# Kernel optimization log

Hardware: AMD Instinct MI355X
Metric: run time of the kernel (lower is better)

## Reference

```python
import jax, jax.numpy as jnp
import numpy as np

B, T, D_MODEL = 1, 2048, 2048
N_HEADS, N_KV_HEADS, HEAD_DIM = 32, 8, 64
N_REP = N_HEADS // N_KV_HEADS
ROPE_THETA = 10000.0


def setup_inputs() -> dict:
    key = jax.random.key(0)
    ks = jax.random.split(key, 5)
    x = jax.random.normal(ks[0], (B, T, D_MODEL), dtype=jnp.float32)
    # rotary frequencies: complex exp stored as (cos, sin) pairs -> [T, HEAD_DIM//2, 2]
    inv_freq = 1.0 / (ROPE_THETA ** (jnp.arange(0, HEAD_DIM, 2, dtype=jnp.float32) / HEAD_DIM))
    angles = jnp.arange(T, dtype=jnp.float32)[:, None] * inv_freq[None, :]  # [T, HEAD_DIM//2]
    freqs_cis = jnp.stack([jnp.cos(angles), jnp.sin(angles)], axis=-1)  # [T, HD/2, 2]
    s = 1.0 / np.sqrt(D_MODEL)
    wq = jax.random.normal(ks[1], (D_MODEL, N_HEADS * HEAD_DIM), dtype=jnp.float32) * s
    wk = jax.random.normal(ks[2], (D_MODEL, N_KV_HEADS * HEAD_DIM), dtype=jnp.float32) * s
    wv = jax.random.normal(ks[3], (D_MODEL, N_KV_HEADS * HEAD_DIM), dtype=jnp.float32) * s
    wo = jax.random.normal(ks[4], (N_HEADS * HEAD_DIM, D_MODEL), dtype=jnp.float32) * (1.0 / np.sqrt(N_HEADS * HEAD_DIM))
    return {"x": x, "freqs_cis": freqs_cis, "wq": wq, "wk": wk, "wv": wv, "wo": wo}


def _apply_rotary(t, freqs_cis):
    # t: [B, T, H, D]; freqs_cis: [T, D//2, 2] as (cos, sin). Complex multiply.
    tr = t.astype(jnp.float32).reshape(*t.shape[:-1], -1, 2)  # [B,T,H,D/2,2]
    re, im = tr[..., 0], tr[..., 1]
    cos = freqs_cis[None, :, None, :, 0]  # [1,T,1,D/2]
    sin = freqs_cis[None, :, None, :, 1]
    out_re = re * cos - im * sin
    out_im = re * sin + im * cos
    out = jnp.stack([out_re, out_im], axis=-1).reshape(t.shape)
    return out.astype(t.dtype)


def reference(x, freqs_cis, wq, wk, wv, wo):
    Bx, Tx, _ = x.shape
    q = (x @ wq).reshape(Bx, Tx, N_HEADS, HEAD_DIM)
    k = (x @ wk).reshape(Bx, Tx, N_KV_HEADS, HEAD_DIM)
    v = (x @ wv).reshape(Bx, Tx, N_KV_HEADS, HEAD_DIM)
    q = _apply_rotary(q, freqs_cis)
    k = _apply_rotary(k, freqs_cis)
    # GQA: group query heads, broadcast against kv heads (no repeat materialization)
    qg = q.transpose(0, 2, 1, 3).reshape(Bx, N_KV_HEADS, N_REP, Tx, HEAD_DIM)  # [B,G,R,T,D]
    kg = k.transpose(0, 2, 1, 3)  # [B,G,T,D]
    vg = v.transpose(0, 2, 1, 3)  # [B,G,T,D]
    scale = 1.0 / np.sqrt(HEAD_DIM)
    scores = jnp.einsum('bgrtd,bgsd->bgrts', qg, kg) * scale  # [B,G,R,T,T]
    causal = jnp.tril(jnp.ones((Tx, Tx), dtype=bool))
    scores = jnp.where(causal, scores, jnp.finfo(scores.dtype).min)
    p = jax.nn.softmax(scores, axis=-1)
    y = jnp.einsum('bgrts,bgsd->bgrtd', p, vg)  # [B,G,R,T,D]
    y = y.reshape(Bx, N_HEADS, Tx, HEAD_DIM).transpose(0, 2, 1, 3).reshape(Bx, Tx, N_HEADS * HEAD_DIM)
    return y @ wo
```

## Files before the change

### kernel.cpp

```cpp
#include <hip/hip_runtime.h>
#include <hip/hip_bf16.h>
#include <stdint.h>
#include <stddef.h>

#define T_SEQ 2048
#define DMODEL 2048
#define NHEADS 32
#define NKV 8
#define HD 64
#define NQD (NHEADS * HD)
#define NKVD (NKV * HD)
#define QKVN (NQD + 2 * NKVD)

typedef __bf16 bf16_t;
typedef __bf16 bf16x8 __attribute__((ext_vector_type(8)));
typedef __bf16 bf16x4 __attribute__((ext_vector_type(4)));
typedef __bf16 bf16x2 __attribute__((ext_vector_type(2)));
typedef float f32x4 __attribute__((ext_vector_type(4)));

typedef __attribute__((address_space(1))) void gvoid_t;
typedef __attribute__((address_space(3))) void lvoid_t;

__device__ __forceinline__ void gload_lds16(const void* g, void* l) {
  __builtin_amdgcn_global_load_lds((gvoid_t*)g, (lvoid_t*)l, 16, 0, 0);
}

__global__ __launch_bounds__(256) void cast_f32_bf16_kernel(
    const float* __restrict__ in, bf16_t* __restrict__ out, int n8) {
  int i = blockIdx.x * 256 + threadIdx.x;
  if (i >= n8) return;
  const float4* p = (const float4*)in + (size_t)i * 2;
  float4 a = p[0], b = p[1];
  bf16x8 o = {(bf16_t)a.x, (bf16_t)a.y, (bf16_t)a.z, (bf16_t)a.w,
              (bf16_t)b.x, (bf16_t)b.y, (bf16_t)b.z, (bf16_t)b.w};
  *(bf16x8*)(out + (size_t)i * 8) = o;
}

__global__ __launch_bounds__(256) void transpose_cast_kernel(
    const float* __restrict__ in, bf16_t* __restrict__ out,
    int R, int C, int ldin, int ldout) {
  __shared__ float tile[32][33];
  const int c0 = blockIdx.x * 32, r0 = blockIdx.y * 32;
  const int tx = threadIdx.x & 31, ty = threadIdx.x >> 5;
#pragma unroll
  for (int i = 0; i < 32; i += 8)
    tile[ty + i][tx] = in[(size_t)(r0 + ty + i) * ldin + c0 + tx];
  __syncthreads();
#pragma unroll
  for (int i = 0; i < 32; i += 8)
    out[(size_t)(c0 + ty + i) * ldout + r0 + tx] = (bf16_t)tile[tx][ty + i];
}

__global__ __launch_bounds__(256) void rope_cast_kernel(
    const float* __restrict__ src, const float* __restrict__ fc,
    bf16_t* __restrict__ dst, int H, int ldin, float oscale) {
  const int i = blockIdx.x * 256 + threadIdx.x;
  const int npr = H * 32;
  const int t = i / npr;
  const int rem = i - t * npr;
  const int h = rem >> 5, fi = rem & 31;
  const float2 rein = *(const float2*)&src[(size_t)t * ldin + h * 64 + fi * 2];
  const float2 cs = *(const float2*)&fc[((size_t)t * 32 + fi) * 2];
  const float o0 = (rein.x * cs.x - rein.y * cs.y) * oscale;
  const float o1 = (rein.x * cs.y + rein.y * cs.x) * oscale;
  bf16x2 ob = {(bf16_t)o0, (bf16_t)o1};
  *(bf16x2*)&dst[(size_t)t * (H * 64) + h * 64 + fi * 2] = ob;
}

__global__ __launch_bounds__(256) void gemm_bt64_kernel(
    const bf16_t* __restrict__ A, const bf16_t* __restrict__ BT,
    float* __restrict__ C, int M, int N, int K) {
  __shared__ bf16_t As[128 * 64];
  __shared__ bf16_t Bs[64 * 64];
  const int tid = threadIdx.x;
  const int lane = tid & 63;
  const int w = tid >> 6;
  const int lr = lane & 15, lg = lane >> 4;
  const int m0 = blockIdx.y * 128, n0 = blockIdx.x * 64;
  const int wm = (w >> 1) * 64, wn = (w & 1) * 32;

  const bf16_t* gA[4];
  bf16_t* lA[4];
#pragma unroll
  for (int j = 0; j < 4; ++j) {
    const int c = tid + j * 256;
    const int row = c >> 3, cc = c & 7;
    gA[j] = A + (size_t)(m0 + row) * K + ((cc ^ (row & 7)) * 8);
    lA[j] = As + c * 8;
  }
  const bf16_t* gB[2];
  bf16_t* lB[2];
#pragma unroll
  for (int j = 0; j < 2; ++j) {
    const int c = tid + j * 256;
    const int row = c >> 3, cc = c & 7;
    gB[j] = BT + (size_t)(n0 + row) * K + ((cc ^ (row & 7)) * 8);
    lB[j] = Bs + c * 8;
  }

  f32x4 acc[4][2] = {};

  for (int k0 = 0; k0 < K; k0 += 64) {
#pragma unroll
    for (int j = 0; j < 4; ++j) gload_lds16(gA[j] + k0, lA[j]);
#pragma unroll
    for (int j = 0; j < 2; ++j) gload_lds16(gB[j] + k0, lB[j]);
    __syncthreads();
#pragma unroll
    for (int ks = 0; ks < 2; ++ks) {
      bf16x8 af[4], bfr[2];
#pragma unroll
      for (int mi = 0; mi < 4; ++mi) {
        const int row = wm + mi * 16 + lr;
        af[mi] = *(const bf16x8*)((const char*)As + row * 128 +
                                  ((ks * 64 + lg * 16) ^ ((row & 7) << 4)));
      }
#pragma unroll
      for (int nj = 0; nj < 2; ++nj) {
        const int row = wn + nj * 16 + lr;
        bfr[nj] = *(const bf16x8*)((const char*)Bs + row * 128 +
                                   ((ks * 64 + lg * 16) ^ ((row & 7) << 4)));
      }
      __builtin_amdgcn_s_setprio(1);
#pragma unroll
      for (int mi = 0; mi < 4; ++mi)
#pragma unroll
        for (int nj = 0; nj < 2; ++nj)
          acc[mi][nj] = __builtin_amdgcn_mfma_f32_16x16x32_bf16(
              af[mi], bfr[nj], acc[mi][nj], 0, 0, 0);
      __builtin_amdgcn_s_setprio(0);
    }
    __syncthreads();
  }

#pragma unroll
  for (int mi = 0; mi < 4; ++mi)
#pragma unroll
    for (int nj = 0; nj < 2; ++nj) {
      const int row = m0 + wm + mi * 16 + lg * 4;
      const int col = n0 + wn + nj * 16 + lr;
#pragma unroll
      for (int r = 0; r < 4; ++r)
        C[(size_t)(row + r) * N + col] = acc[mi][nj][r];
    }
}

__global__ __launch_bounds__(256) void attn_kernel(
    const bf16_t* __restrict__ Q, const bf16_t* __restrict__ Kb,
    const bf16_t* __restrict__ VT, bf16_t* __restrict__ Y,
    bf16_t* __restrict__ Yp, float* __restrict__ Mb, float* __restrict__ Lb) {
  __shared__ bf16_t Ks[2][64 * 64];
  __shared__ bf16_t Vs[2][64 * 64];
  __shared__ char Pb[4][32 * 128];
  const int bid = blockIdx.x;
  const int kh = bid & 7;
  const int idx = 95 - (bid >> 3);
  int qt, c;
  if (idx < 32) { qt = idx; c = 0; }
  else { const int t2 = idx - 32; qt = 32 + (t2 >> 1); c = t2 & 1; }
  const int nt = (qt + 2) >> 1;
  const bool single = (nt <= 16);
  const int tstart = c * 16;
  const int tend = (c == 0) ? (single ? nt : 16) : nt;

  const int tid = threadIdx.x, lane = tid & 63, w = tid >> 6;
  const int h = kh * 4 + w;
  const int lr = lane & 15, lg = lane >> 4;
  const int q0 = qt * 32;
  char* pb = (char*)Pb[w];
  const int swz = (lr & 7) << 4;

  const int rA = w * 8 + (lane >> 3);
  const int rB = (w + 4) * 8 + (lane >> 3);
  const int ce = (((lane & 7) ^ (lane >> 3)) * 8);
  const bf16_t* kgA = Kb + (size_t)rA * NKVD + kh * HD + ce;
  const bf16_t* kgB = Kb + (size_t)rB * NKVD + kh * HD + ce;
  const bf16_t* vgA = VT + (size_t)(kh * HD + rA) * T_SEQ + ce;
  const bf16_t* vgB = VT + (size_t)(kh * HD + rB) * T_SEQ + ce;
  const int ldA = w * 512 + lane * 8;
  const int ldB = (w + 4) * 512 + lane * 8;

  bf16x8 qf[2][2];
#pragma unroll
  for (int iq = 0; iq < 2; ++iq)
#pragma unroll
    for (int ks = 0; ks < 2; ++ks)
      qf[iq][ks] = *(const bf16x8*)&Q[(size_t)(q0 + iq * 16 + lr) * NQD + h * HD + ks * 32 + lg * 8];

  float m_i[2] = {-1e30f, -1e30f}, l_i[2] = {0.f, 0.f};
  f32x4 acc_o[2][4] = {};

  {
    const size_t ko = (size_t)tstart * 64 * NKVD;
    gload_lds16(kgA + ko, &Ks[0][ldA]);
    gload_lds16(kgB + ko, &Ks[0][ldB]);
    gload_lds16(vgA + tstart * 64, &Vs[0][ldA]);
    gload_lds16(vgB + tstart * 64, &Vs[0][ldB]);
  }
  __syncthreads();

  int cur = 0;
  for (int t = tstart; t < tend; ++t) {
    const int s0 = t * 64;
    if (t + 1 < tend) {
      const size_t ko = (size_t)(s0 + 64) * NKVD;
      gload_lds16(kgA + ko, &Ks[cur ^ 1][ldA]);
      gload_lds16(kgB + ko, &Ks[cur ^ 1][ldB]);
      gload_lds16(vgA + s0 + 64, &Vs[cur ^ 1][ldA]);
      gload_lds16(vgB + s0 + 64, &Vs[cur ^ 1][ldB]);
    }
    const char* kbase = (const char*)&Ks[cur][0];
    const char* vbase = (const char*)&Vs[cur][0];

    bf16x8 kf[4][2];
#pragma unroll
    for (int j = 0; j < 4; ++j)
#pragma unroll
      for (int ks = 0; ks < 2; ++ks)
        kf[j][ks] = *(const bf16x8*)(kbase + (j * 16 + lr) * 128 + ((ks * 64 + lg * 16) ^ swz));

    f32x4 st[2][4] = {};
    __builtin_amdgcn_s_setprio(1);
#pragma unroll
    for (int iq = 0; iq < 2; ++iq)
#pragma unroll
      for (int j = 0; j < 4; ++j)
#pragma unroll
        for (int ks = 0; ks < 2; ++ks)
          st[iq][j] = __builtin_amdgcn_mfma_f32_16x16x32_bf16(kf[j][ks], qf[iq][ks], st[iq][j], 0, 0, 0);
    __builtin_amdgcn_s_setprio(0);

    bf16x8 vf[2][4];
#pragma unroll
    for (int ks = 0; ks < 2; ++ks)
#pragma unroll
      for (int df = 0; df < 4; ++df)
        vf[ks][df] = *(const bf16x8*)(vbase + (df * 16 + lr) * 128 + ((ks * 64 + lg * 16) ^ swz));

    const bool domask = (s0 + 64 > q0);
#pragma unroll
    for (int iq = 0; iq < 2; ++iq) {
      float sv[16];
      const int tq = q0 + iq * 16 + lr;
#pragma unroll
      for (int j = 0; j < 4; ++j)
#pragma unroll
        for (int r = 0; r < 4; ++r) {
          float v = st[iq][j][r];
          if (domask && (s0 + j * 16 + lg * 4 + r > tq)) v = -1e30f;
          sv[j * 4 + r] = v;
        }
      float pm = fmaxf(fmaxf(fmaxf(sv[0], sv[1]), fmaxf(sv[2], sv[3])),
                       fmaxf(fmaxf(sv[4], sv[5]), fmaxf(sv[6], sv[7])));
      float pm2 = fmaxf(fmaxf(fmaxf(sv[8], sv[9]), fmaxf(sv[10], sv[11])),
                        fmaxf(fmaxf(sv[12], sv[13]), fmaxf(sv[14], sv[15])));
      pm = fmaxf(pm, pm2);
      pm = fmaxf(pm, __shfl_xor(pm, 16));
      pm = fmaxf(pm, __shfl_xor(pm, 32));

      if (!__all(pm <= m_i[iq] + 8.0f)) {
        const float mnew = fmaxf(m_i[iq], pm);
        const float es = exp2f(m_i[iq] - mnew);
        m_i[iq] = mnew;
        l_i[iq] *= es;
        float eso[4];
#pragma unroll
        for (int r = 0; r < 4; ++r) eso[r] = __shfl(es, lg * 4 + r);
#pragma unroll
        for (int df = 0; df < 4; ++df)
#pragma unroll
          for (int r = 0; r < 4; ++r) acc_o[iq][df][r] *= eso[r];
      }

      float rs0 = 0.f, rs1 = 0.f;
      bf16_t pe[16];
#pragma unroll
      for (int z = 0; z < 8; ++z) {
        const float p = exp2f(sv[z] - m_i[iq]);
        rs0 += p;
        pe[z] = (bf16_t)p;
      }
#pragma unroll
      for (int z = 8; z < 16; ++z) {
        const float p = exp2f(sv[z] - m_i[iq]);
        rs1 += p;
        pe[z] = (bf16_t)p;
      }
      l_i[iq] += rs0 + rs1;

#pragma unroll
      for (int j = 0; j < 4; ++j) {
        bf16x4 pk = {pe[j * 4 + 0], pe[j * 4 + 1], pe[j * 4 + 2], pe[j * 4 + 3]};
        *(bf16x4*)(pb + (iq * 16 + lr) * 128 + ((j * 32 + lg * 8) ^ swz)) = pk;
      }
    }

    bf16x8 pa[2][2];
#pragma unroll
    for (int iq = 0; iq < 2; ++iq)
#pragma unroll
      for (int ks = 0; ks < 2; ++ks)
        pa[iq][ks] = *(const bf16x8*)(pb + (iq * 16 + lr) * 128 + ((ks * 64 + lg * 16) ^ swz));

    __builtin_amdgcn_s_setprio(1);
#pragma unroll
    for (int iq = 0; iq < 2; ++iq)
#pragma unroll
      for (int df = 0; df < 4; ++df)
#pragma unroll
        for (int ks = 0; ks < 2; ++ks)
          acc_o[iq][df] = __builtin_amdgcn_mfma_f32_16x16x32_bf16(pa[iq][ks], vf[ks][df], acc_o[iq][df], 0, 0, 0);
    __builtin_amdgcn_s_setprio(0);

    __syncthreads();
    cur ^= 1;
  }

  float lts[2];
#pragma unroll
  for (int iq = 0; iq < 2; ++iq) {
    float lt = l_i[iq];
    lt += __shfl_xor(lt, 16);
    lt += __shfl_xor(lt, 32);
    lts[iq] = lt;
  }
  if (single) {
#pragma unroll
    for (int iq = 0; iq < 2; ++iq) {
      float lf[4];
#pragma unroll
      for (int r = 0; r < 4; ++r) lf[r] = __shfl(lts[iq], lg * 4 + r);
#pragma unroll
      for (int r = 0; r < 4; ++r) {
        const float inv = 1.f / lf[r];
        const int t = q0 + iq * 16 + lg * 4 + r;
#pragma unroll
        for (int df = 0; df < 4; ++df)
          Y[(size_t)t * NQD + h * HD + df * 16 + lr] = (bf16_t)(acc_o[iq][df][r] * inv);
      }
    }
  } else {
    const int cid = (kh * 32 + (qt - 32)) * 2 + c;
    bf16_t* yp = Yp + ((size_t)cid * 4 + w) * 2048;
#pragma unroll
    for (int iq = 0; iq < 2; ++iq) {
      float lf[4];
#pragma unroll
      for (int r = 0; r < 4; ++r) lf[r] = __shfl(lts[iq], lg * 4 + r);
#pragma unroll
      for (int r = 0; r < 4; ++r) {
        const float inv = 1.f / lf[r];
        const int q = iq * 16 + lg * 4 + r;
#pragma unroll
        for (int df = 0; df < 4; ++df)
          yp[q * 64 + df * 16 + lr] = (bf16_t)(acc_o[iq][df][r] * inv);
      }
    }
    if (lg == 0) {
#pragma unroll
      for (int iq = 0; iq < 2; ++iq) {
        Mb[cid * 128 + w * 32 + iq * 16 + lr] = m_i[iq];
        Lb[cid * 128 + w * 32 + iq * 16 + lr] = lts[iq];
      }
    }
  }
}

__global__ __launch_bounds__(256) void merge_kernel(
    const bf16_t* __restrict__ Yp, const float* __restrict__ Mb,
    const float* __restrict__ Lb, bf16_t* __restrict__ Y) {
  const int qt = 32 + blockIdx.x, kh = blockIdx.y;
  const int w = threadIdx.x >> 6, lane = threadIdx.x & 63;
  const int h = kh * 4 + w;
  const int cid0 = (kh * 32 + (qt - 32)) * 2, cid1 = cid0 + 1;
  const bf16_t* y0 = Yp + ((size_t)cid0 * 4 + w) * 2048;
  const bf16_t* y1 = Yp + ((size_t)cid1 * 4 + w) * 2048;
#pragma unroll 4
  for (int q = 0; q < 32; ++q) {
    const float m0 = Mb[cid0 * 128 + w * 32 + q];
    const float m1 = Mb[cid1 * 128 + w * 32 + q];
    const float l0 = Lb[cid0 * 128 + w * 32 + q];
    const float l1 = Lb[cid1 * 128 + w * 32 + q];
    const float M = fmaxf(m0, m1);
    const float a0 = exp2f(m0 - M) * l0;
    const float a1 = exp2f(m1 - M) * l1;
    const float inv = 1.f / (a0 + a1);
    const float v0 = (float)y0[q * 64 + lane];
    const float v1 = (float)y1[q * 64 + lane];
    Y[(size_t)(qt * 32 + q) * NQD + h * HD + lane] = (bf16_t)((v0 * a0 + v1 * a1) * inv);
  }
}

extern "C" void kernel_launch(void* const* d_in, const int* in_sizes, int n_in,
                              void* d_out, int out_size, void* d_ws, size_t ws_size,
                              hipStream_t stream) {
  const float* x = (const float*)d_in[0];
  const float* fc = (const float*)d_in[1];
  const float* wq = (const float*)d_in[2];
  const float* wk = (const float*)d_in[3];
  const float* wv = (const float*)d_in[4];
  const float* wo = (const float*)d_in[5];
  float* out = (float*)d_out;
  char* ws = (char*)d_ws;

  bf16_t* xb   = (bf16_t*)(ws + 0);
  bf16_t* wT   = (bf16_t*)(ws + (8u << 20));
  float*  qkvf = (float*)(ws + (20u << 20));
  bf16_t* qb   = (bf16_t*)(ws + (8u << 20));
  bf16_t* kb   = (bf16_t*)(ws + (16u << 20));
  bf16_t* vt   = (bf16_t*)(ws + (18u << 20));
  bf16_t* woT  = (bf16_t*)(ws + (20u << 20));
  bf16_t* yb   = (bf16_t*)(ws + 0);
  bf16_t* Yp   = (bf16_t*)(ws + (28u << 20));
  float*  Mb   = (float*)(ws + (36u << 20));
  float*  Lb   = (float*)(ws + (36u << 20) + (256u << 10));

  const float SCL_Q = 0.18033688011112042f;

  hipLaunchKernelGGL(cast_f32_bf16_kernel, dim3(2048), dim3(256), 0, stream,
                     x, xb, (T_SEQ * DMODEL) / 8);
  hipLaunchKernelGGL(transpose_cast_kernel, dim3(64, 64), dim3(256), 0, stream,
                     wq, wT, DMODEL, NQD, NQD, DMODEL);
  hipLaunchKernelGGL(transpose_cast_kernel, dim3(16, 64), dim3(256), 0, stream,
                     wk, wT + (size_t)NQD * DMODEL, DMODEL, NKVD, NKVD, DMODEL);
  hipLaunchKernelGGL(transpose_cast_kernel, dim3(16, 64), dim3(256), 0, stream,
                     wv, wT + (size_t)(NQD + NKVD) * DMODEL, DMODEL, NKVD, NKVD, DMODEL);
  hipLaunchKernelGGL(gemm_bt64_kernel, dim3(QKVN / 64, T_SEQ / 128), dim3(256), 0, stream,
                     xb, wT, qkvf, T_SEQ, QKVN, DMODEL);
  hipLaunchKernelGGL(rope_cast_kernel, dim3((T_SEQ * NHEADS * 32) / 256), dim3(256), 0, stream,
                     qkvf, fc, qb, NHEADS, QKVN, SCL_Q);
  hipLaunchKernelGGL(rope_cast_kernel, dim3((T_SEQ * NKV * 32) / 256), dim3(256), 0, stream,
                     qkvf + NQD, fc, kb, NKV, QKVN, 1.0f);
  hipLaunchKernelGGL(transpose_cast_kernel, dim3(16, 64), dim3(256), 0, stream,
                     qkvf + NQD + NKVD, vt, T_SEQ, NKVD, QKVN, T_SEQ);
  hipLaunchKernelGGL(transpose_cast_kernel, dim3(64, 64), dim3(256), 0, stream,
                     wo, woT, NQD, DMODEL, DMODEL, NQD);
  hipLaunchKernelGGL(attn_kernel, dim3(768), dim3(256), 0, stream,
                     qb, kb, vt, yb, Yp, Mb, Lb);
  hipLaunchKernelGGL(merge_kernel, dim3(32, 8), dim3(256), 0, stream,
                     Yp, Mb, Lb, yb);
  hipLaunchKernelGGL(gemm_bt64_kernel, dim3(DMODEL / 64, T_SEQ / 128), dim3(256), 0, stream,
                     yb, woT, out, T_SEQ, DMODEL, NQD);
}
```

Baseline: 184.7 us.

## Rebalance causal attention split into 1/2/3 chunks and load V directly from global

Reworks the attention work decomposition so long query tiles are split into three KV chunks, mid tiles into two, and short tiles run whole, with the merge kernel extended to combine up to three partials. V fragments are now read straight from global memory into registers instead of being staged through LDS, which halves shared memory and allows a launch-bounds occupancy hint of four blocks. The partial output buffer is moved into the output tensor, which is later overwritten by the final GEMM. This targets the tail imbalance of causal attention and LDS pressure, at the cost of uncached strided global V reads and more merge work.

After: 258.2 us. 39.8% more time.

```diff
diff --git a/kernel.cpp b/kernel.cpp
--- a/kernel.cpp
+++ b/kernel.cpp
@@ -145,23 +145,23 @@
     }
 }
 
-__global__ __launch_bounds__(256) void attn_kernel(
+__global__ __launch_bounds__(256, 4) void attn_kernel(
     const bf16_t* __restrict__ Q, const bf16_t* __restrict__ Kb,
     const bf16_t* __restrict__ VT, bf16_t* __restrict__ Y,
     bf16_t* __restrict__ Yp, float* __restrict__ Mb, float* __restrict__ Lb) {
   __shared__ bf16_t Ks[2][64 * 64];
-  __shared__ bf16_t Vs[2][64 * 64];
   __shared__ char Pb[4][32 * 128];
   const int bid = blockIdx.x;
   const int kh = bid & 7;
-  const int idx = 95 - (bid >> 3);
-  int qt, c;
-  if (idx < 32) { qt = idx; c = 0; }
-  else { const int t2 = idx - 32; qt = 32 + (t2 >> 1); c = t2 & 1; }
+  const int item = bid >> 3;
+  int qt, c, nc;
+  if (item < 75) { qt = 63 - item / 3; c = item % 3; nc = 3; }
+  else if (item < 115) { const int j = item - 75; qt = 38 - (j >> 1); c = j & 1; nc = 2; }
+  else { qt = 18 - (item - 115); c = 0; nc = 1; }
   const int nt = (qt + 2) >> 1;
-  const bool single = (nt <= 16);
-  const int tstart = c * 16;
-  const int tend = (c == 0) ? (single ? nt : 16) : nt;
+  const int tstart = (nt * c) / nc;
+  const int tend = (nt * (c + 1)) / nc;
+  const bool single = (nc == 1);
 
   const int tid = threadIdx.x, lane = tid & 63, w = tid >> 6;
   const int h = kh * 4 + w;
@@ -170,15 +170,17 @@
   char* pb = (char*)Pb[w];
   const int swz = (lr & 7) << 4;
 
-  const int rA = w * 8 + (lane >> 3);
-  const int rB = (w + 4) * 8 + (lane >> 3);
-  const int ce = (((lane & 7) ^ (lane >> 3)) * 8);
-  const bf16_t* kgA = Kb + (size_t)rA * NKVD + kh * HD + ce;
-  const bf16_t* kgB = Kb + (size_t)rB * NKVD + kh * HD + ce;
-  const bf16_t* vgA = VT + (size_t)(kh * HD + rA) * T_SEQ + ce;
-  const bf16_t* vgB = VT + (size_t)(kh * HD + rB) * T_SEQ + ce;
-  const int ldA = w * 512 + lane * 8;
-  const int ldB = (w + 4) * 512 + lane * 8;
+  const int r1 = tid >> 3, cc1 = tid & 7;
+  const int r2 = r1 + 32;
+  const bf16_t* kg1 = Kb + (size_t)r1 * NKVD + kh * HD + ((cc1 ^ (r1 & 7)) * 8);
+  const bf16_t* kg2 = Kb + (size_t)r2 * NKVD + kh * HD + ((cc1 ^ (r2 & 7)) * 8);
+  const int ld1 = tid * 8, ld2 = tid * 8 + 2048;
+  const size_t kstep = (size_t)64 * NKVD;
+
+  const bf16_t* vp0 = VT + (size_t)(kh * HD + 0 + lr) * T_SEQ + lg * 8 + tstart * 64;
+  const bf16_t* vp1 = VT + (size_t)(kh * HD + 16 + lr) * T_SEQ + lg * 8 + tstart * 64;
+  const bf16_t* vp2 = VT + (size_t)(kh * HD + 32 + lr) * T_SEQ + lg * 8 + tstart * 64;
+  const bf16_t* vp3 = VT + (size_t)(kh * HD + 48 + lr) * T_SEQ + lg * 8 + tstart * 64;
 
   bf16x8 qf[2][2];
 #pragma unroll
@@ -189,29 +191,33 @@
 
   float m_i[2] = {-1e30f, -1e30f}, l_i[2] = {0.f, 0.f};
   f32x4 acc_o[2][4] = {};
-
-  {
-    const size_t ko = (size_t)tstart * 64 * NKVD;
-    gload_lds16(kgA + ko, &Ks[0][ldA]);
-    gload_lds16(kgB + ko, &Ks[0][ldB]);
-    gload_lds16(vgA + tstart * 64, &Vs[0][ldA]);
-    gload_lds16(vgB + tstart * 64, &Vs[0][ldB]);
-  }
+  const f32x4 Z = {0.f, 0.f, 0.f, 0.f};
+
+  size_t koff = (size_t)tstart * kstep;
+  gload_lds16(kg1 + koff, &Ks[0][ld1]);
+  gload_lds16(kg2 + koff, &Ks[0][ld2]);
   __syncthreads();
 
   int cur = 0;
   for (int t = tstart; t < tend; ++t) {
     const int s0 = t * 64;
     if (t + 1 < tend) {
-      const size_t ko = (size_t)(s0 + 64) * NKVD;
-      gload_lds16(kgA + ko, &Ks[cur ^ 1][ldA]);
-      gload_lds16(kgB + ko, &Ks[cur ^ 1][ldB]);
-      gload_lds16(vgA + s0 + 64, &Vs[cur ^ 1][ldA]);
-      gload_lds16(vgB + s0 + 64, &Vs[cur ^ 1][ldB]);
-    }
+      gload_lds16(kg1 + koff + kstep, &Ks[cur ^ 1][ld1]);
+      gload_lds16(kg2 + koff + kstep, &Ks[cur ^ 1][ld2]);
+    }
+    koff += kstep;
+
+    bf16x8 vf[2][4];
+#pragma unroll
+    for (int ks = 0; ks < 2; ++ks) {
+      vf[ks][0] = *(const bf16x8*)(vp0 + ks * 32);
+      vf[ks][1] = *(const bf16x8*)(vp1 + ks * 32);
+      vf[ks][2] = *(const bf16x8*)(vp2 + ks * 32);
+      vf[ks][3] = *(const bf16x8*)(vp3 + ks * 32);
+    }
+    vp0 += 64; vp1 += 64; vp2 += 64; vp3 += 64;
+
     const char* kbase = (const char*)&Ks[cur][0];
-    const char* vbase = (const char*)&Vs[cur][0];
-
     bf16x8 kf[4][2];
 #pragma unroll
     for (int j = 0; j < 4; ++j)
@@ -219,23 +225,16 @@
       for (int ks = 0; ks < 2; ++ks)
         kf[j][ks] = *(const bf16x8*)(kbase + (j * 16 + lr) * 128 + ((ks * 64 + lg * 16) ^ swz));
 
-    f32x4 st[2][4] = {};
+    f32x4 st[2][4];
     __builtin_amdgcn_s_setprio(1);
 #pragma unroll
     for (int iq = 0; iq < 2; ++iq)
 #pragma unroll
-      for (int j = 0; j < 4; ++j)
-#pragma unroll
-        for (int ks = 0; ks < 2; ++ks)
-          st[iq][j] = __builtin_amdgcn_mfma_f32_16x16x32_bf16(kf[j][ks], qf[iq][ks], st[iq][j], 0, 0, 0);
+      for (int j = 0; j < 4; ++j) {
+        st[iq][j] = __builtin_amdgcn_mfma_f32_16x16x32_bf16(kf[j][0], qf[iq][0], Z, 0, 0, 0);
+        st[iq][j] = __builtin_amdgcn_mfma_f32_16x16x32_bf16(kf[j][1], qf[iq][1], st[iq][j], 0, 0, 0);
+      }
     __builtin_amdgcn_s_setprio(0);
-
-    bf16x8 vf[2][4];
-#pragma unroll
-    for (int ks = 0; ks < 2; ++ks)
-#pragma unroll
-      for (int df = 0; df < 4; ++df)
-        vf[ks][df] = *(const bf16x8*)(vbase + (df * 16 + lr) * 128 + ((ks * 64 + lg * 16) ^ swz));
 
     const bool domask = (s0 + 64 > q0);
 #pragma unroll
@@ -340,7 +339,8 @@
       }
     }
   } else {
-    const int cid = (kh * 32 + (qt - 32)) * 2 + c;
+    const int cid = (nc == 3) ? (kh * 115 + 40 + (qt - 39) * 3 + c)
+                              : (kh * 115 + (qt - 19) * 2 + c);
     bf16_t* yp = Yp + ((size_t)cid * 4 + w) * 2048;
 #pragma unroll
     for (int iq = 0; iq < 2; ++iq) {
@@ -369,25 +369,34 @@
 __global__ __launch_bounds__(256) void merge_kernel(
     const bf16_t* __restrict__ Yp, const float* __restrict__ Mb,
     const float* __restrict__ Lb, bf16_t* __restrict__ Y) {
-  const int qt = 32 + blockIdx.x, kh = blockIdx.y;
+  const int qt = 19 + blockIdx.x, kh = blockIdx.y;
   const int w = threadIdx.x >> 6, lane = threadIdx.x & 63;
   const int h = kh * 4 + w;
-  const int cid0 = (kh * 32 + (qt - 32)) * 2, cid1 = cid0 + 1;
-  const bf16_t* y0 = Yp + ((size_t)cid0 * 4 + w) * 2048;
-  const bf16_t* y1 = Yp + ((size_t)cid1 * 4 + w) * 2048;
+  const int nc = (qt < 39) ? 2 : 3;
+  const int base = (qt < 39) ? (kh * 115 + (qt - 19) * 2)
+                             : (kh * 115 + 40 + (qt - 39) * 3);
+  const bf16_t* y0 = Yp + ((size_t)(base + 0) * 4 + w) * 2048;
+  const bf16_t* y1 = Yp + ((size_t)(base + 1) * 4 + w) * 2048;
+  const bf16_t* y2 = Yp + ((size_t)(base + 2) * 4 + w) * 2048;
 #pragma unroll 4
   for (int q = 0; q < 32; ++q) {
-    const float m0 = Mb[cid0 * 128 + w * 32 + q];
-    const float m1 = Mb[cid1 * 128 + w * 32 + q];
-    const float l0 = Lb[cid0 * 128 + w * 32 + q];
-    const float l1 = Lb[cid1 * 128 + w * 32 + q];
-    const float M = fmaxf(m0, m1);
+    const float m0 = Mb[(base + 0) * 128 + w * 32 + q];
+    const float m1 = Mb[(base + 1) * 128 + w * 32 + q];
+    const float l0 = Lb[(base + 0) * 128 + w * 32 + q];
+    const float l1 = Lb[(base + 1) * 128 + w * 32 + q];
+    float m2 = -1e30f, l2 = 0.f;
+    if (nc == 3) {
+      m2 = Mb[(base + 2) * 128 + w * 32 + q];
+      l2 = Lb[(base + 2) * 128 + w * 32 + q];
+    }
+    const float M = fmaxf(fmaxf(m0, m1), m2);
     const float a0 = exp2f(m0 - M) * l0;
     const float a1 = exp2f(m1 - M) * l1;
-    const float inv = 1.f / (a0 + a1);
-    const float v0 = (float)y0[q * 64 + lane];
-    const float v1 = (float)y1[q * 64 + lane];
-    Y[(size_t)(qt * 32 + q) * NQD + h * HD + lane] = (bf16_t)((v0 * a0 + v1 * a1) * inv);
+    const float a2 = (nc == 3) ? exp2f(m2 - M) * l2 : 0.f;
+    const float inv = 1.f / (a0 + a1 + a2);
+    float v = (float)y0[q * 64 + lane] * a0 + (float)y1[q * 64 + lane] * a1;
+    if (nc == 3) v += (float)y2[q * 64 + lane] * a2;
+    Y[(size_t)(qt * 32 + q) * NQD + h * HD + lane] = (bf16_t)(v * inv);
   }
 }
 
@@ -411,9 +420,9 @@
   bf16_t* vt   = (bf16_t*)(ws + (18u << 20));
   bf16_t* woT  = (bf16_t*)(ws + (20u << 20));
   bf16_t* yb   = (bf16_t*)(ws + 0);
-  bf16_t* Yp   = (bf16_t*)(ws + (28u << 20));
-  float*  Mb   = (float*)(ws + (36u << 20));
-  float*  Lb   = (float*)(ws + (36u << 20) + (256u << 10));
+  float*  Mb   = (float*)(ws + (28u << 20));
+  float*  Lb   = (float*)(ws + (29u << 20));
+  bf16_t* Yp   = (bf16_t*)d_out;
 
   const float SCL_Q = 0.18033688011112042f;
 
@@ -435,9 +444,9 @@
                      qkvf + NQD + NKVD, vt, T_SEQ, NKVD, QKVN, T_SEQ);
   hipLaunchKernelGGL(transpose_cast_kernel, dim3(64, 64), dim3(256), 0, stream,
                      wo, woT, NQD, DMODEL, DMODEL, NQD);
-  hipLaunchKernelGGL(attn_kernel, dim3(768), dim3(256), 0, stream,
+  hipLaunchKernelGGL(attn_kernel, dim3(134 * 8), dim3(256), 0, stream,
                      qb, kb, vt, yb, Yp, Mb, Lb);
-  hipLaunchKernelGGL(merge_kernel, dim3(32, 8), dim3(256), 0, stream,
+  hipLaunchKernelGGL(merge_kernel, dim3(45, 8), dim3(256), 0, stream,
                      Yp, Mb, Lb, yb);
   hipLaunchKernelGGL(gemm_bt64_kernel, dim3(DMODEL / 64, T_SEQ / 128), dim3(256), 0, stream,
                      yb, woT, out, T_SEQ, DMODEL, NQD);
```
